# Optimization experiments

Hardware: AMD Instinct MI355X
Metric: run time of the kernel (lower is better)

Reference implementation:

```python
import jax, jax.numpy as jnp
import numpy as np

B, TQ, TP, D = 4, 512, 512, 256


def setup_inputs() -> dict:
    key = jax.random.key(0)
    ks = jax.random.split(key, 5)
    return {
        "q": jax.random.normal(ks[0], (B, TQ, D), dtype=jnp.float32),
        "p": jax.random.normal(ks[1], (B, TP, D), dtype=jnp.float32),
        "W0": jax.random.normal(ks[2], (D, D), dtype=jnp.float32) / np.sqrt(D),
        "W1": jax.random.normal(ks[3], (D, D), dtype=jnp.float32) / np.sqrt(D),
        "vc": jax.random.normal(ks[4], (D, 1), dtype=jnp.float32) * 0.05,
    }


def reference(q, p, W0, W1, vc):
    # q: [B,Tq,Dq], p: [B,Tp,Dp]
    prod_q = jnp.einsum('bqd,de->bqe', q, W0)   # [B,Tq,dim]
    prod_p = jnp.einsum('bpd,de->bpe', p, W1)   # [B,Tp,dim]
    # additive attention energies: tanh over broadcast sum [B,Tp,Tq,dim]
    energy = jnp.tanh(prod_p[:, :, None, :] + prod_q[:, None, :, :])
    scores = jnp.einsum('bpqe,e->bpq', energy, vc[:, 0])  # [B,Tp,Tq]
    # original softmax is over axis=-2 of [B,Tp,Tq], i.e. the Tp axis
    weights = jax.nn.softmax(scores, axis=1)   # [B,Tp,Tq]
    # weighted sum over the Tq axis of (tiled) q
    attention_q = jnp.einsum('bpq,bqd->bpd', weights, q)  # [B,Tp,Dq]
    return attention_q
```

## Files before the change

kernel.cpp:

```cpp
#include <hip/hip_runtime.h>

#define NB 4
#define TT 512
#define DD 256
#define K2L2E    2.885390081777927f
#define NEG2L2E (-2.885390081777927f)

#if defined(__has_builtin)
# if __has_builtin(__builtin_amdgcn_global_load_lds)
#  define HAS_GLL 1
# endif
#endif

typedef float v2f __attribute__((ext_vector_type(2)));

__device__ __forceinline__ v2f pk_fma(v2f a, v2f b, v2f c) {
#if defined(__has_builtin)
# if __has_builtin(__builtin_elementwise_fma)
    return __builtin_elementwise_fma(a, b, c);
# else
    v2f r; r.x = __builtin_fmaf(a.x, b.x, c.x); r.y = __builtin_fmaf(a.y, b.y, c.y); return r;
# endif
#else
    v2f r; r.x = __builtin_fmaf(a.x, b.x, c.x); r.y = __builtin_fmaf(a.y, b.y, c.y); return r;
#endif
}
__device__ __forceinline__ v2f splat2(float s) { v2f r; r.x = s; r.y = s; return r; }

__device__ __forceinline__ void stage16(const float* __restrict__ g, float* l) {
#ifdef HAS_GLL
    __builtin_amdgcn_global_load_lds((const __attribute__((address_space(1))) void*)g,
                                     (__attribute__((address_space(3))) void*)l, 16, 0, 0);
#else
    *(float4*)l = *(const float4*)g;
#endif
}

__global__ __launch_bounds__(256) void proj_exp_kernel(
    const float* __restrict__ qin, const float* __restrict__ pin,
    const float* __restrict__ W0, const float* __restrict__ W1,
    float* __restrict__ expQ, float* __restrict__ expP)
{
    const int blk = blockIdx.x;
    const int wh = blk >> 8, tid = blk & 255;
    const int m0 = (tid >> 2) * 32, n0 = (tid & 3) * 64;
    const float* A = wh ? pin : qin;
    const float* W = wh ? W1 : W0;

    __shared__ __align__(16) float As[32 * 34];
    __shared__ __align__(16) float Bs[32 * 64];

    const int t  = threadIdx.x;
    const int ar = t >> 3, ac4 = (t & 7) * 4;
    const int br = t >> 4, bc4 = (t & 15) * 4;
    const int tm = wh ? (t >> 4) : (t & 15);
    const int tn = wh ? (t & 15) : (t >> 4);

    const float* Ap = A + (long)(m0 + ar) * DD + ac4;

    float4 av  = *(const float4*)Ap;
    float4 bv0 = *(const float4*)(W + (long)br * DD + n0 + bc4);
    float4 bv1 = *(const float4*)(W + (long)(br + 16) * DD + n0 + bc4);

    v2f accv[2][2];
    accv[0][0] = splat2(0.f); accv[0][1] = splat2(0.f);
    accv[1][0] = splat2(0.f); accv[1][1] = splat2(0.f);

    for (int c = 0; c < 8; ++c) {
        As[(ac4 + 0) * 34 + ar] = av.x;
        As[(ac4 + 1) * 34 + ar] = av.y;
        As[(ac4 + 2) * 34 + ar] = av.z;
        As[(ac4 + 3) * 34 + ar] = av.w;
        *(float4*)&Bs[br * 64 + bc4]        = bv0;
        *(float4*)&Bs[(br + 16) * 64 + bc4] = bv1;
        __syncthreads();
        if (c < 7) {
            int k1 = (c + 1) * 32;
            av  = *(const float4*)(Ap + k1);
            bv0 = *(const float4*)(W + (long)(k1 + br) * DD + n0 + bc4);
            bv1 = *(const float4*)(W + (long)(k1 + 16 + br) * DD + n0 + bc4);
        }
        #pragma unroll
        for (int kk = 0; kk < 32; ++kk) {
            float2 a = *(const float2*)&As[kk * 34 + 2 * tm];
            float4 b = *(const float4*)&Bs[kk * 64 + 4 * tn];
            v2f b01; b01.x = b.x; b01.y = b.y;
            v2f b23; b23.x = b.z; b23.y = b.w;
            accv[0][0] = pk_fma(splat2(a.x), b01, accv[0][0]);
            accv[0][1] = pk_fma(splat2(a.x), b23, accv[0][1]);
            accv[1][0] = pk_fma(splat2(a.y), b01, accv[1][0]);
            accv[1][1] = pk_fma(splat2(a.y), b23, accv[1][1]);
        }
        __syncthreads();
    }

    float acc[2][4];
    #pragma unroll
    for (int i = 0; i < 2; ++i) {
        acc[i][0] = accv[i][0].x; acc[i][1] = accv[i][0].y;
        acc[i][2] = accv[i][1].x; acc[i][3] = accv[i][1].y;
    }

    const int bi = m0 >> 9;
    const int ml = m0 & 511;
    if (wh) {
        #pragma unroll
        for (int i = 0; i < 2; ++i) {
            float4 st;
            st.x = __builtin_amdgcn_exp2f(acc[i][0] * K2L2E);
            st.y = __builtin_amdgcn_exp2f(acc[i][1] * K2L2E);
            st.z = __builtin_amdgcn_exp2f(acc[i][2] * K2L2E);
            st.w = __builtin_amdgcn_exp2f(acc[i][3] * K2L2E);
            *(float4*)(expP + ((long)bi * TT + ml + 2 * tm + i) * DD + n0 + 4 * tn) = st;
        }
    } else {
        #pragma unroll
        for (int j = 0; j < 4; ++j) {
            int d = n0 + 4 * tn + j;
            float2 st;
            st.x = __builtin_amdgcn_exp2f(acc[0][j] * K2L2E);
            st.y = __builtin_amdgcn_exp2f(acc[1][j] * K2L2E);
            *(float2*)(expQ + ((long)bi * DD + d) * TT + ml + 2 * tm) = st;
        }
    }
}

__global__ __launch_bounds__(512, 6) void score_kernel(
    const float* __restrict__ expP, const float* __restrict__ expQ,
    const float* __restrict__ vc, float* __restrict__ ebuf, float* __restrict__ lpart)
{
    const int b = blockIdx.z, pt = blockIdx.y, qt = blockIdx.x;
    const int p0 = pt * 32, q0 = qt * 64;
    const int t  = threadIdx.x;
    const int qx = t & 31, py = t >> 5;

    __shared__ __align__(16) float PA[32 * 128];
    __shared__ __align__(16) float QB[128 * 64];
    __shared__ __align__(16) float vcs[DD];

    const float* gP = expP + ((long)b * TT + p0) * DD;
    const float* gQ = expQ + (long)b * DD * TT + q0;

    #pragma unroll
    for (int s = 0; s < 2; ++s) {
        int f = t + 512 * s, pr = f >> 5, d4 = (f & 31) * 4;
        stage16(gP + (long)pr * DD + d4, &PA[f * 4]);
    }
    #pragma unroll
    for (int s = 0; s < 4; ++s) {
        int f = t + 512 * s, d = f >> 4, o4 = (f & 15) * 4;
        stage16(gQ + (long)d * TT + o4, &QB[f * 4]);
    }
    if (t < DD) vcs[t] = vc[t];
    __syncthreads();

    v2f acc[2]; acc[0] = splat2(0.f); acc[1] = splat2(0.f);
    const v2f one = splat2(1.0f);

    for (int c = 0; c < 2; ++c) {
        if (c == 1) {
            __syncthreads();
            #pragma unroll
            for (int s = 0; s < 2; ++s) {
                int f = t + 512 * s, pr = f >> 5, d4 = (f & 31) * 4;
                stage16(gP + (long)pr * DD + 128 + d4, &PA[f * 4]);
            }
            #pragma unroll
            for (int s = 0; s < 4; ++s) {
                int f = t + 512 * s, d = f >> 4, o4 = (f & 15) * 4;
                stage16(gQ + (long)(128 + d) * TT + o4, &QB[f * 4]);
            }
            __syncthreads();
        }
        const float* vcb = &vcs[c * 128];
        #pragma unroll 4
        for (int dq = 0; dq < 32; ++dq) {
            float4 vq = *(const float4*)&vcb[4 * dq];
            float4 aq0 = *(const float4*)&PA[(2 * py) * 128 + 4 * dq];
            float4 aq1 = *(const float4*)&PA[(2 * py + 1) * 128 + 4 * dq];
            v2f B0 = *(const v2f*)&QB[(4 * dq + 0) * 64 + 2 * qx];
            v2f B1 = *(const v2f*)&QB[(4 * dq + 1) * 64 + 2 * qx];
            v2f B2 = *(const v2f*)&QB[(4 * dq + 2) * 64 + 2 * qx];
            v2f B3 = *(const v2f*)&QB[(4 * dq + 3) * 64 + 2 * qx];
            #pragma unroll
            for (int i = 0; i < 2; ++i) {
                float4 a = i ? aq1 : aq0;
                v2f f0 = pk_fma(splat2(a.x), B0, one);
                v2f f1 = pk_fma(splat2(a.y), B1, one);
                v2f f2 = pk_fma(splat2(a.z), B2, one);
                v2f f3 = pk_fma(splat2(a.w), B3, one);
                v2f t01 = f0 * f1;
                v2f t23 = f2 * f3;
                v2f den = t01 * t23;
                v2f n01 = pk_fma(splat2(vq.x), f1, splat2(vq.y) * f0);
                v2f n23 = pk_fma(splat2(vq.z), f3, splat2(vq.w) * f2);
                v2f num = pk_fma(n01, t23, n23 * t01);
                v2f r;
                r.x = __builtin_amdgcn_rcpf(den.x);
                r.y = __builtin_amdgcn_rcpf(den.y);
                acc[i] = pk_fma(num, r, acc[i]);
            }
        }
    }

    float* eb = ebuf + ((long)b * TT + p0) * TT + q0;
    v2f colp = splat2(0.f);
    #pragma unroll
    for (int i = 0; i < 2; ++i) {
        float2 ev;
        ev.x = __builtin_amdgcn_exp2f(acc[i].x * NEG2L2E);
        ev.y = __builtin_amdgcn_exp2f(acc[i].y * NEG2L2E);
        *(float2*)(eb + (long)(2 * py + i) * TT + 2 * qx) = ev;
        colp.x += ev.x; colp.y += ev.y;
    }
    __syncthreads();
    float* scr = (float*)&PA[0];
    *(float2*)&scr[py * 64 + 2 * qx] = make_float2(colp.x, colp.y);
    __syncthreads();
    if (t < 64) {
        float s = 0.f;
        #pragma unroll
        for (int r = 0; r < 16; ++r) s += scr[r * 64 + t];
        lpart[((long)b * 16 + pt) * TT + q0 + t] = s;
    }
}

__global__ __launch_bounds__(256) void out_kernel(
    const float* __restrict__ ebuf, const float* __restrict__ qin,
    const float* __restrict__ lpart, float* __restrict__ out)
{
    const int b = blockIdx.z, pt = blockIdx.y, dt = blockIdx.x;
    const int m0 = pt * 32, n0 = dt * 32;
    const int t    = threadIdx.x;
    const int wv   = t >> 6;
    const int lane = t & 63;
    const int pg   = lane >> 3;
    const int dg   = lane & 7;

    __shared__ __align__(16) float smem[4 * 32 * 36];
    __shared__ float linv[TT];
    float* As = smem;
    float* Bs = smem + 64 * 36;

    #pragma unroll
    for (int s = 0; s < 2; ++s) {
        int qq = t + 256 * s;
        float sum = 0.f;
        #pragma unroll
        for (int pb = 0; pb < 16; ++pb) sum += lpart[((long)b * 16 + pb) * TT + qq];
        linv[qq] = __builtin_amdgcn_rcpf(sum);
    }
    __syncthreads();

    const float* Ab = ebuf + ((long)b * TT + m0) * TT;
    const float* Bb = qin + (long)b * TT * DD + n0;

    const int ar = t >> 3, ak4 = (t & 7) * 4;

    v2f acc[4][2];
    #pragma unroll
    for (int i = 0; i < 4; ++i) { acc[i][0] = splat2(0.f); acc[i][1] = splat2(0.f); }

    for (int c = 0; c < 8; ++c) {
        const int k0 = c * 64;
        #pragma unroll
        for (int s = 0; s < 2; ++s) {
            int f = t + 256 * s, kr = f >> 3, d4 = (f & 7) * 4;
            stage16(Bb + (long)(k0 + kr) * DD + d4, &Bs[f * 4]);
        }
        #pragma unroll
        for (int s = 0; s < 2; ++s) {
            int kq = ak4 + 32 * s;
            float4 a = *(const float4*)(Ab + (long)ar * TT + k0 + kq);
            float4 lv = *(const float4*)&linv[k0 + kq];
            As[(kq + 0) * 36 + ar] = a.x * lv.x;
            As[(kq + 1) * 36 + ar] = a.y * lv.y;
            As[(kq + 2) * 36 + ar] = a.z * lv.z;
            As[(kq + 3) * 36 + ar] = a.w * lv.w;
        }
        __syncthreads();
        const int kb = 16 * wv;
        #pragma unroll
        for (int u = 0; u < 16; ++u) {
            int kk = kb + u;
            float4 a  = *(const float4*)&As[kk * 36 + 4 * pg];
            float4 bq = *(const float4*)&Bs[kk * 32 + 4 * dg];
            v2f b0; b0.x = bq.x; b0.y = bq.y;
            v2f b1; b1.x = bq.z; b1.y = bq.w;
            acc[0][0] = pk_fma(splat2(a.x), b0, acc[0][0]);
            acc[0][1] = pk_fma(splat2(a.x), b1, acc[0][1]);
            acc[1][0] = pk_fma(splat2(a.y), b0, acc[1][0]);
            acc[1][1] = pk_fma(splat2(a.y), b1, acc[1][1]);
            acc[2][0] = pk_fma(splat2(a.z), b0, acc[2][0]);
            acc[2][1] = pk_fma(splat2(a.z), b1, acc[2][1]);
            acc[3][0] = pk_fma(splat2(a.w), b0, acc[3][0]);
            acc[3][1] = pk_fma(splat2(a.w), b1, acc[3][1]);
        }
        __syncthreads();
    }

    float* scr = smem;
    #pragma unroll
    for (int i = 0; i < 4; ++i) {
        *(v2f*)&scr[wv * 1152 + (4 * pg + i) * 36 + 4 * dg]     = acc[i][0];
        *(v2f*)&scr[wv * 1152 + (4 * pg + i) * 36 + 4 * dg + 2] = acc[i][1];
    }
    __syncthreads();
    {
        int pr = t >> 3, d0 = (t & 7) * 4;
        float4 s0 = *(const float4*)&scr[0 * 1152 + pr * 36 + d0];
        float4 s1 = *(const float4*)&scr[1 * 1152 + pr * 36 + d0];
        float4 s2 = *(const float4*)&scr[2 * 1152 + pr * 36 + d0];
        float4 s3 = *(const float4*)&scr[3 * 1152 + pr * 36 + d0];
        float4 v;
        v.x = (s0.x + s1.x) + (s2.x + s3.x);
        v.y = (s0.y + s1.y) + (s2.y + s3.y);
        v.z = (s0.z + s1.z) + (s2.z + s3.z);
        v.w = (s0.w + s1.w) + (s2.w + s3.w);
        *(float4*)(out + ((long)b * TT + m0 + pr) * DD + n0 + d0) = v;
    }
}

extern "C" void kernel_launch(void* const* d_in, const int* in_sizes, int n_in,
                              void* d_out, int out_size, void* d_ws, size_t ws_size,
                              hipStream_t stream) {
    const float* q  = (const float*)d_in[0];
    const float* p  = (const float*)d_in[1];
    const float* W0 = (const float*)d_in[2];
    const float* W1 = (const float*)d_in[3];
    const float* vc = (const float*)d_in[4];
    float* out = (float*)d_out;

    float* ws    = (float*)d_ws;
    float* expQ  = ws;
    float* expP  = ws + 524288;
    float* ebuf  = ws + 1048576;
    float* lpart = ws + 2097152;

    proj_exp_kernel<<<dim3(512), 256, 0, stream>>>(q, p, W0, W1, expQ, expP);
    score_kernel<<<dim3(8, 16, NB), 512, 0, stream>>>(expP, expQ, vc, ebuf, lpart);
    out_kernel<<<dim3(8, 16, NB), 256, 0, stream>>>(ebuf, q, lpart, out);
}
```

Baseline: 118.5 us.

## Enlarge projection GEMM tile to 64x64 with 4x4 per-thread outputs

The projection kernel now computes 64x64 output tiles with a K-chunk of 64, giving each thread a 4x4 micro-tile instead of 2x4 and halving the grid to 256 blocks. W tiles are staged straight into LDS with global_load_lds, and the register double-buffered prefetch is dropped. This is meant to raise arithmetic intensity per LDS read and cut redundant global loads. The trade-offs are fewer blocks on a 256-CU device, more LDS per block and no overlap of loads with compute.

```diff
diff --git a/kernel.cpp b/kernel.cpp
--- a/kernel.cpp
+++ b/kernel.cpp
@@ -42,85 +42,83 @@
     float* __restrict__ expQ, float* __restrict__ expP)
 {
     const int blk = blockIdx.x;
-    const int wh = blk >> 8, tid = blk & 255;
-    const int m0 = (tid >> 2) * 32, n0 = (tid & 3) * 64;
+    const int wh  = blk >> 7, tid = blk & 127;
+    const int m0 = (tid >> 2) * 64, n0 = (tid & 3) * 64;
     const float* A = wh ? pin : qin;
     const float* W = wh ? W1 : W0;
 
-    __shared__ __align__(16) float As[32 * 34];
-    __shared__ __align__(16) float Bs[32 * 64];
+    __shared__ __align__(16) float As[64 * 68];
+    __shared__ __align__(16) float Bs[64 * 64];
 
     const int t  = threadIdx.x;
-    const int ar = t >> 3, ac4 = (t & 7) * 4;
-    const int br = t >> 4, bc4 = (t & 15) * 4;
-    const int tm = wh ? (t >> 4) : (t & 15);
-    const int tn = wh ? (t & 15) : (t >> 4);
-
-    const float* Ap = A + (long)(m0 + ar) * DD + ac4;
-
-    float4 av  = *(const float4*)Ap;
-    float4 bv0 = *(const float4*)(W + (long)br * DD + n0 + bc4);
-    float4 bv1 = *(const float4*)(W + (long)(br + 16) * DD + n0 + bc4);
-
-    v2f accv[2][2];
-    accv[0][0] = splat2(0.f); accv[0][1] = splat2(0.f);
-    accv[1][0] = splat2(0.f); accv[1][1] = splat2(0.f);
-
-    for (int c = 0; c < 8; ++c) {
-        As[(ac4 + 0) * 34 + ar] = av.x;
-        As[(ac4 + 1) * 34 + ar] = av.y;
-        As[(ac4 + 2) * 34 + ar] = av.z;
-        As[(ac4 + 3) * 34 + ar] = av.w;
-        *(float4*)&Bs[br * 64 + bc4]        = bv0;
-        *(float4*)&Bs[(br + 16) * 64 + bc4] = bv1;
+    const int tm = t & 15, tn = t >> 4;
+
+    v2f acc[4][2];
+    #pragma unroll
+    for (int i = 0; i < 4; ++i) { acc[i][0] = splat2(0.f); acc[i][1] = splat2(0.f); }
+
+    for (int c = 0; c < 4; ++c) {
+        const int k0 = c * 64;
+        #pragma unroll
+        for (int s = 0; s < 4; ++s) {
+            int f = t + 256 * s, kr = f >> 4, c4 = (f & 15) * 4;
+            stage16(W + (long)(k0 + kr) * DD + n0 + c4, &Bs[f * 4]);
+        }
+        #pragma unroll
+        for (int s = 0; s < 4; ++s) {
+            int f = t + 256 * s, mr = f >> 4, c4 = (f & 15) * 4;
+            float4 a = *(const float4*)(A + (long)(m0 + mr) * DD + k0 + c4);
+            As[(c4 + 0) * 68 + mr] = a.x;
+            As[(c4 + 1) * 68 + mr] = a.y;
+            As[(c4 + 2) * 68 + mr] = a.z;
+            As[(c4 + 3) * 68 + mr] = a.w;
+        }
         __syncthreads();
-        if (c < 7) {
-            int k1 = (c + 1) * 32;
-            av  = *(const float4*)(Ap + k1);
-            bv0 = *(const float4*)(W + (long)(k1 + br) * DD + n0 + bc4);
-            bv1 = *(const float4*)(W + (long)(k1 + 16 + br) * DD + n0 + bc4);
-        }
-        #pragma unroll
-        for (int kk = 0; kk < 32; ++kk) {
-            float2 a = *(const float2*)&As[kk * 34 + 2 * tm];
+        #pragma unroll
+        for (int kk = 0; kk < 64; ++kk) {
+            float4 a = *(const float4*)&As[kk * 68 + 4 * tm];
             float4 b = *(const float4*)&Bs[kk * 64 + 4 * tn];
             v2f b01; b01.x = b.x; b01.y = b.y;
             v2f b23; b23.x = b.z; b23.y = b.w;
-            accv[0][0] = pk_fma(splat2(a.x), b01, accv[0][0]);
-            accv[0][1] = pk_fma(splat2(a.x), b23, accv[0][1]);
-            accv[1][0] = pk_fma(splat2(a.y), b01, accv[1][0]);
-            accv[1][1] = pk_fma(splat2(a.y), b23, accv[1][1]);
+            acc[0][0] = pk_fma(splat2(a.x), b01, acc[0][0]);
+            acc[0][1] = pk_fma(splat2(a.x), b23, acc[0][1]);
+            acc[1][0] = pk_fma(splat2(a.y), b01, acc[1][0]);
+            acc[1][1] = pk_fma(splat2(a.y), b23, acc[1][1]);
+            acc[2][0] = pk_fma(splat2(a.z), b01, acc[2][0]);
+            acc[2][1] = pk_fma(splat2(a.z), b23, acc[2][1]);
+            acc[3][0] = pk_fma(splat2(a.w), b01, acc[3][0]);
+            acc[3][1] = pk_fma(splat2(a.w), b23, acc[3][1]);
         }
         __syncthreads();
-    }
-
-    float acc[2][4];
-    #pragma unroll
-    for (int i = 0; i < 2; ++i) {
-        acc[i][0] = accv[i][0].x; acc[i][1] = accv[i][0].y;
-        acc[i][2] = accv[i][1].x; acc[i][3] = accv[i][1].y;
     }
 
     const int bi = m0 >> 9;
     const int ml = m0 & 511;
     if (wh) {
         #pragma unroll
-        for (int i = 0; i < 2; ++i) {
+        for (int i = 0; i < 4; ++i) {
             float4 st;
-            st.x = __builtin_amdgcn_exp2f(acc[i][0] * K2L2E);
-            st.y = __builtin_amdgcn_exp2f(acc[i][1] * K2L2E);
-            st.z = __builtin_amdgcn_exp2f(acc[i][2] * K2L2E);
-            st.w = __builtin_amdgcn_exp2f(acc[i][3] * K2L2E);
-            *(float4*)(expP + ((long)bi * TT + ml + 2 * tm + i) * DD + n0 + 4 * tn) = st;
+            st.x = __builtin_amdgcn_exp2f(acc[i][0].x * K2L2E);
+            st.y = __builtin_amdgcn_exp2f(acc[i][0].y * K2L2E);
+            st.z = __builtin_amdgcn_exp2f(acc[i][1].x * K2L2E);
+            st.w = __builtin_amdgcn_exp2f(acc[i][1].y * K2L2E);
+            *(float4*)(expP + ((long)bi * TT + ml + 4 * tm + i) * DD + n0 + 4 * tn) = st;
         }
     } else {
         #pragma unroll
         for (int j = 0; j < 4; ++j) {
+            float aj[4];
+            aj[0] = (j < 2) ? ((j & 1) ? acc[0][0].y : acc[0][0].x) : ((j & 1) ? acc[0][1].y : acc[0][1].x);
+            aj[1] = (j < 2) ? ((j & 1) ? acc[1][0].y : acc[1][0].x) : ((j & 1) ? acc[1][1].y : acc[1][1].x);
+            aj[2] = (j < 2) ? ((j & 1) ? acc[2][0].y : acc[2][0].x) : ((j & 1) ? acc[2][1].y : acc[2][1].x);
+            aj[3] = (j < 2) ? ((j & 1) ? acc[3][0].y : acc[3][0].x) : ((j & 1) ? acc[3][1].y : acc[3][1].x);
+            float4 st;
+            st.x = __builtin_amdgcn_exp2f(aj[0] * K2L2E);
+            st.y = __builtin_amdgcn_exp2f(aj[1] * K2L2E);
+            st.z = __builtin_amdgcn_exp2f(aj[2] * K2L2E);
+            st.w = __builtin_amdgcn_exp2f(aj[3] * K2L2E);
             int d = n0 + 4 * tn + j;
-            float2 st;
-            st.x = __builtin_amdgcn_exp2f(acc[0][j] * K2L2E);
-            st.y = __builtin_amdgcn_exp2f(acc[1][j] * K2L2E);
-            *(float2*)(expQ + ((long)bi * DD + d) * TT + ml + 2 * tm) = st;
+            *(float4*)(expQ + ((long)bi * DD + d) * TT + ml + 4 * tm) = st;
         }
     }
 }
@@ -337,7 +335,7 @@
     float* ebuf  = ws + 1048576;
     float* lpart = ws + 2097152;
 
-    proj_exp_kernel<<<dim3(512), 256, 0, stream>>>(q, p, W0, W1, expQ, expP);
+    proj_exp_kernel<<<dim3(256), 256, 0, stream>>>(q, p, W0, W1, expQ, expP);
     score_kernel<<<dim3(8, 16, NB), 512, 0, stream>>>(expP, expQ, vc, ebuf, lpart);
     out_kernel<<<dim3(8, 16, NB), 256, 0, stream>>>(ebuf, q, lpart, out);
 }
```

New measurement: 122.2 us. 3.1% more time.
